# Kernel tuning notes

Measured on AMD Instinct MI355X. Metric: run time of the kernel, lower is better.

## Reference

```python
import jax, jax.numpy as jnp
import numpy as np

SINKHORN_ALPHA = 20.0
WEIGHT_LOSS_ECR = 100.0
OT_MAX_ITER = 100
STOP_THR = 0.005
EPS = 1e-16


def setup_inputs() -> dict:
    key = jax.random.key(0)
    # cost matrix: [num_topics, vocab]
    M = jax.random.uniform(key, (512, 65536), dtype=jnp.float32)
    return {"M": M}


def reference(M) -> jnp.ndarray:
    n, m = M.shape
    a = jnp.full((n, 1), 1.0 / n, dtype=M.dtype)   # row marginal
    b = jnp.full((m, 1), 1.0 / m, dtype=M.dtype)   # col marginal
    u0 = jnp.full((n, 1), 1.0 / n, dtype=M.dtype)
    K = jnp.exp(-M * SINKHORN_ALPHA)               # [n, m]

    def cond_fn(carry):
        u, v, err, cpt = carry
        return (err > STOP_THR) & (cpt < OT_MAX_ITER)

    def body_fn(carry):
        u, v, err, cpt = carry
        v = b / (K.T @ u + EPS)                    # [m, 1]
        u = a / (K @ v + EPS)                      # [n, 1]
        cpt = cpt + 1
        # convergence check every 50 iters (cpt % 50 == 1), matching torch loop
        err = jax.lax.cond(
            cpt % 50 == 1,
            lambda: jnp.sum(jnp.abs(v * (K.T @ u) - b)).astype(err.dtype),
            lambda: err,
        )
        return (u, v, err, cpt)

    init = (u0, jnp.zeros((m, 1), dtype=M.dtype), jnp.asarray(1.0, M.dtype), jnp.asarray(0, jnp.int32))
    u, v, _, _ = jax.lax.while_loop(cond_fn, body_fn, init)

    transp = u * (K * v.T)                         # [n, m] transport plan
    loss_ECR = jnp.sum(transp * M) * WEIGHT_LOSS_ECR
    return loss_ECR
```

## Files before the change

### kernel.cpp

```cpp
#include <hip/hip_runtime.h>
#include <hip/hip_cooperative_groups.h>

namespace cg = cooperative_groups;

#define NROW 512
#define NCOL 65536
#define BANDS 8
#define BPB   128

static __device__ __forceinline__ float wave_sum(float x) {
  #pragma unroll
  for (int off = 32; off; off >>= 1) x += __shfl_down(x, off, 64);
  return x;
}

__global__ __launch_bounds__(256)
void k1a_partial(const float* __restrict__ M, float* __restrict__ tPart,
                 float* __restrict__ eA) {
  const int tid = threadIdx.x, bid = blockIdx.x;
  const int band = bid >> 7, blk = bid & 127;
  const int chunk = tid & 127;
  const int part  = tid >> 7;
  const int col0  = (blk << 9) + (chunk << 2);
  const int r0    = (band << 6) + (part << 5);

  __shared__ float sCol[2 * 512];

  if (bid == 0 && tid < 3) eA[tid] = 0.f;

  float4 cs = {0.f, 0.f, 0.f, 0.f};
  #pragma unroll 8
  for (int r = r0; r < r0 + 32; ++r) {
    float4 m = *(const float4*)(M + (size_t)r * NCOL + col0);
    cs.x += __expf(-20.f * m.x);
    cs.y += __expf(-20.f * m.y);
    cs.z += __expf(-20.f * m.z);
    cs.w += __expf(-20.f * m.w);
  }
  *(float4*)(sCol + part * 512 + (chunk << 2)) = cs;
  __syncthreads();
  if (tid < 128) {
    float4 a = *(const float4*)(sCol + (tid << 2));
    float4 b = *(const float4*)(sCol + 512 + (tid << 2));
    float4 t = {a.x + b.x, a.y + b.y, a.z + b.z, a.w + b.w};
    *(float4*)(tPart + (size_t)band * NCOL + (blk << 9) + (tid << 2)) = t;
  }
}

__global__ __launch_bounds__(256)
void k1b_v1(const float* __restrict__ tPart, float* __restrict__ v) {
  const int gid = blockIdx.x * 256 + threadIdx.x;
  const int col0 = gid << 2;
  const float am = 1.0f / NROW, bm = 1.0f / NCOL, EPSV = 1e-16f;
  float4 t = {0.f, 0.f, 0.f, 0.f};
  #pragma unroll
  for (int b = 0; b < BANDS; ++b) {
    float4 p = *(const float4*)(tPart + (size_t)b * NCOL + col0);
    t.x += p.x; t.y += p.y; t.z += p.z; t.w += p.w;
  }
  float4 vv = {bm / (t.x * am + EPSV), bm / (t.y * am + EPSV),
               bm / (t.z * am + EPSV), bm / (t.w * am + EPSV)};
  *(float4*)(v + col0) = vv;
}

__global__ __launch_bounds__(256)
void k2_rowdot(const float* __restrict__ M, const float* __restrict__ v,
               float* __restrict__ u) {
  const int tid = threadIdx.x, row = blockIdx.x;
  const float am = 1.0f / NROW, EPSV = 1e-16f;
  const float4* M4 = (const float4*)M + (size_t)row * (NCOL / 4);
  const float4* V4 = (const float4*)v;
  __shared__ float sRed[4];

  float acc = 0.f;
  #pragma unroll 8
  for (int it = 0; it < NCOL / 4 / 256; ++it) {
    const int c = (it << 8) + tid;
    float4 m = M4[c];
    float4 vv = V4[c];
    acc += __expf(-20.f * m.x) * vv.x + __expf(-20.f * m.y) * vv.y
         + __expf(-20.f * m.z) * vv.z + __expf(-20.f * m.w) * vv.w;
  }
  acc = wave_sum(acc);
  if ((tid & 63) == 0) sRed[tid >> 6] = acc;
  __syncthreads();
  if (tid == 0)
    u[row] = am / (sRed[0] + sRed[1] + sRed[2] + sRed[3] + EPSV);
}

__global__ __launch_bounds__(256)
void k3a_partial(const float* __restrict__ M, const float* __restrict__ v,
                 const float* __restrict__ u, float* __restrict__ tPart,
                 float* __restrict__ eA) {
  const int tid = threadIdx.x, bid = blockIdx.x;
  const int band = bid >> 7, blk = bid & 127;
  const int chunk = tid & 127;
  const int part  = tid >> 7;
  const int col0  = (blk << 9) + (chunk << 2);
  const int r0l   = part << 5;

  __shared__ float sU[64];
  __shared__ float sCol[2 * 512];
  __shared__ float sRed[4];

  if (tid < 64) sU[tid] = u[(band << 6) + tid];
  __syncthreads();

  const float4 vv = *(const float4*)(v + col0);
  const float* Mb = M + (size_t)(band << 6) * NCOL;
  float4 cs = {0.f, 0.f, 0.f, 0.f};
  float lacc = 0.f;
  #pragma unroll 8
  for (int rl = r0l; rl < r0l + 32; ++rl) {
    float4 m = *(const float4*)(Mb + (size_t)rl * NCOL + col0);
    float e0 = __expf(-20.f * m.x), e1 = __expf(-20.f * m.y);
    float e2 = __expf(-20.f * m.z), e3 = __expf(-20.f * m.w);
    float us = sU[rl];
    cs.x = fmaf(e0, us, cs.x);
    cs.y = fmaf(e1, us, cs.y);
    cs.z = fmaf(e2, us, cs.z);
    cs.w = fmaf(e3, us, cs.w);
    lacc += us * (e0 * m.x * vv.x + e1 * m.y * vv.y
                + e2 * m.z * vv.z + e3 * m.w * vv.w);
  }
  *(float4*)(sCol + part * 512 + (chunk << 2)) = cs;
  lacc = wave_sum(lacc);
  if ((tid & 63) == 0) sRed[tid >> 6] = lacc;
  __syncthreads();
  if (tid < 128) {
    float4 a = *(const float4*)(sCol + (tid << 2));
    float4 b = *(const float4*)(sCol + 512 + (tid << 2));
    float4 t = {a.x + b.x, a.y + b.y, a.z + b.z, a.w + b.w};
    *(float4*)(tPart + (size_t)band * NCOL + (blk << 9) + (tid << 2)) = t;
  }
  if (tid == 0)
    atomicAdd(&eA[2], sRed[0] + sRed[1] + sRed[2] + sRed[3]);
}

__global__ __launch_bounds__(256)
void k3b_err(const float* __restrict__ tPart, const float* __restrict__ v,
             float* __restrict__ tArr, float* __restrict__ eA) {
  const int tid = threadIdx.x;
  const int gid = blockIdx.x * 256 + tid;
  const int col0 = gid << 2;
  const float bm = 1.0f / NCOL;
  __shared__ float sRed[4];

  float4 t = {0.f, 0.f, 0.f, 0.f};
  #pragma unroll
  for (int b = 0; b < BANDS; ++b) {
    float4 p = *(const float4*)(tPart + (size_t)b * NCOL + col0);
    t.x += p.x; t.y += p.y; t.z += p.z; t.w += p.w;
  }
  *(float4*)(tArr + col0) = t;
  float4 vv = *(const float4*)(v + col0);
  float pe = fabsf(vv.x * t.x - bm) + fabsf(vv.y * t.y - bm)
           + fabsf(vv.z * t.z - bm) + fabsf(vv.w * t.w - bm);
  pe = wave_sum(pe);
  if ((tid & 63) == 0) sRed[tid >> 6] = pe;
  __syncthreads();
  if (tid == 0)
    atomicAdd(&eA[0], sRed[0] + sRed[1] + sRed[2] + sRed[3]);
}

__global__ void k4_decide(const float* __restrict__ eA, float* __restrict__ out,
                          int* __restrict__ done) {
  if (threadIdx.x == 0) {
    if (eA[0] <= 0.005f) { out[0] = 100.f * eA[2]; done[0] = 1; }
    else                 { out[0] = 0.f;           done[0] = 0; }
  }
}

__global__ __launch_bounds__(1024)
void k5_fallback(const float* __restrict__ M, float* __restrict__ out,
                 float* __restrict__ v, float* __restrict__ u,
                 const float* __restrict__ tArr, float* __restrict__ eA,
                 const int* __restrict__ done) {
  if (done[0]) return;
  cg::grid_group grid = cg::this_grid();
  const int tid = threadIdx.x, bid = blockIdx.x;
  const float am = 1.0f / NROW, bm = 1.0f / NCOL, EPSV = 1e-16f;

  __shared__ float sU[NROW];
  __shared__ float sCol[16 * 256];
  __shared__ float sRedA[16], sRedB[16];

  const int chunk = tid & 63;
  const int part  = tid >> 6;
  const int col0  = (bid << 8) + (chunk << 2);
  const int r0    = part << 5;
  const int row0  = bid << 1;

  float tt = (tid < 256) ? tArr[(bid << 8) + tid] : 0.f;

  int cpt = 1;
  while (true) {
    if (tid < 256) v[(bid << 8) + tid] = bm / (tt + EPSV);
    grid.sync();
    cpt++;

    {
      const float4* M40 = (const float4*)M + (size_t)row0 * (NCOL / 4);
      const float4* M41 = (const float4*)M + (size_t)(row0 + 1) * (NCOL / 4);
      const float4* V4  = (const float4*)v;
      float ra = 0.f, rb = 0.f;
      #pragma unroll 4
      for (int it = 0; it < NCOL / 4 / 1024; ++it) {
        const int c = (it << 10) + tid;
        float4 vv = V4[c];
        float4 m0 = M40[c], m1 = M41[c];
        ra += __expf(-20.f * m0.x) * vv.x + __expf(-20.f * m0.y) * vv.y
            + __expf(-20.f * m0.z) * vv.z + __expf(-20.f * m0.w) * vv.w;
        rb += __expf(-20.f * m1.x) * vv.x + __expf(-20.f * m1.y) * vv.y
            + __expf(-20.f * m1.z) * vv.z + __expf(-20.f * m1.w) * vv.w;
      }
      ra = wave_sum(ra); rb = wave_sum(rb);
      if ((tid & 63) == 0) { sRedA[tid >> 6] = ra; sRedB[tid >> 6] = rb; }
      __syncthreads();
      if (tid < 2) {
        const float* sr = (tid == 0) ? sRedA : sRedB;
        float s = 0.f;
        #pragma unroll
        for (int w = 0; w < 16; ++w) s += sr[w];
        u[row0 + tid] = am / (s + EPSV);
      }
    }
    grid.sync();
    if (cpt >= 100) break;

    if (tid < NROW) sU[tid] = u[tid];
    __syncthreads();
    float4 cs = {0.f, 0.f, 0.f, 0.f};
    #pragma unroll 4
    for (int r = r0; r < r0 + 32; ++r) {
      float4 m = *(const float4*)(M + (size_t)r * NCOL + col0);
      float us = sU[r];
      cs.x = fmaf(__expf(-20.f * m.x), us, cs.x);
      cs.y = fmaf(__expf(-20.f * m.y), us, cs.y);
      cs.z = fmaf(__expf(-20.f * m.z), us, cs.z);
      cs.w = fmaf(__expf(-20.f * m.w), us, cs.w);
    }
    *(float4*)(sCol + part * 256 + (chunk << 2)) = cs;
    __syncthreads();
    if (tid < 256) {
      tt = 0.f;
      #pragma unroll
      for (int p = 0; p < 16; ++p) tt += sCol[p * 256 + tid];
    }

    if (cpt == 51) {
      float pe = (tid < 256) ? fabsf(v[(bid << 8) + tid] * tt - bm) : 0.f;
      pe = wave_sum(pe);
      __syncthreads();
      if ((tid & 63) == 0) sRedA[tid >> 6] = pe;
      __syncthreads();
      if (tid == 0) {
        float s = 0.f;
        #pragma unroll
        for (int w = 0; w < 16; ++w) s += sRedA[w];
        atomicAdd(&eA[1], s);
      }
      grid.sync();
      if (eA[1] <= 0.005f) break;
    }
  }

  __syncthreads();
  if (tid < NROW) sU[tid] = u[tid];
  __syncthreads();
  {
    const float4 vv = *(const float4*)(v + col0);
    float lacc = 0.f;
    #pragma unroll 4
    for (int r = r0; r < r0 + 32; ++r) {
      float4 m = *(const float4*)(M + (size_t)r * NCOL + col0);
      float us = sU[r];
      lacc += us * (__expf(-20.f * m.x) * m.x * vv.x
                  + __expf(-20.f * m.y) * m.y * vv.y
                  + __expf(-20.f * m.z) * m.z * vv.z
                  + __expf(-20.f * m.w) * m.w * vv.w);
    }
    lacc = wave_sum(lacc);
    if ((tid & 63) == 0) sRedA[tid >> 6] = lacc;
    __syncthreads();
    if (tid == 0) {
      float s = 0.f;
      #pragma unroll
      for (int w = 0; w < 16; ++w) s += sRedA[w];
      atomicAdd(out, 100.f * s);
    }
  }
}

extern "C" void kernel_launch(void* const* d_in, const int* in_sizes, int n_in,
                              void* d_out, int out_size, void* d_ws, size_t ws_size,
                              hipStream_t stream) {
  const float* M = (const float*)d_in[0];
  float* out = (float*)d_out;

  const size_t offV = 0;
  const size_t offT = offV + (size_t)NCOL * sizeof(float);
  const size_t offU = offT + (size_t)NCOL * sizeof(float);
  const size_t offE = offU + 4096;
  const size_t offD = offE + 256;
  const size_t offP = offD + 256;
  const size_t need = offP + (size_t)BANDS * NCOL * sizeof(float);
  if (ws_size < need) return;

  char* ws = (char*)d_ws;
  float* v     = (float*)(ws + offV);
  float* tArr  = (float*)(ws + offT);
  float* u     = (float*)(ws + offU);
  float* eA    = (float*)(ws + offE);
  int*   done  = (int*)(ws + offD);
  float* tPart = (float*)(ws + offP);

  k1a_partial<<<dim3(1024), dim3(256), 0, stream>>>(M, tPart, eA);
  k1b_v1     <<<dim3(64),   dim3(256), 0, stream>>>(tPart, v);
  k2_rowdot  <<<dim3(512),  dim3(256), 0, stream>>>(M, v, u);
  k3a_partial<<<dim3(1024), dim3(256), 0, stream>>>(M, v, u, tPart, eA);
  k3b_err    <<<dim3(64),   dim3(256), 0, stream>>>(tPart, v, tArr, eA);
  k4_decide  <<<dim3(1),    dim3(64),  0, stream>>>(eA, out, done);

  void* args[] = { (void*)&M, (void*)&out, (void*)&v, (void*)&u,
                   (void*)&tArr, (void*)&eA, (void*)&done };
  hipLaunchCooperativeKernel((void*)k5_fallback, dim3(256), dim3(1024),
                             args, 0, stream);
}
```

Measured before the change: 269.4 us.

## Fuse first Sinkhorn iteration and error check into single cooperative kernel

Replaces the six-kernel prologue (column sums, v init, row dot, partial column sums, error reduction, decide) with phases inside the single cooperative kernel, separated by grid syncs. The ECR loss partial for the early-exit case is folded into the row-dot pass, and the banded partial-sum workspace round trips are dropped. This targets launch overhead and extra global traffic in the common early-converging case. In exchange it adds grid-wide barriers and runs with only 256 blocks of 1024 threads, which may lower memory-level parallelism for the heavy M passes.

```diff
diff --git a/kernel.cpp b/kernel.cpp
--- a/kernel.cpp
+++ b/kernel.cpp
@@ -5,8 +5,6 @@
 
 #define NROW 512
 #define NCOL 65536
-#define BANDS 8
-#define BPB   128
 
 static __device__ __forceinline__ float wave_sum(float x) {
   #pragma unroll
@@ -14,176 +12,17 @@
   return x;
 }
 
-__global__ __launch_bounds__(256)
-void k1a_partial(const float* __restrict__ M, float* __restrict__ tPart,
-                 float* __restrict__ eA) {
-  const int tid = threadIdx.x, bid = blockIdx.x;
-  const int band = bid >> 7, blk = bid & 127;
-  const int chunk = tid & 127;
-  const int part  = tid >> 7;
-  const int col0  = (blk << 9) + (chunk << 2);
-  const int r0    = (band << 6) + (part << 5);
-
-  __shared__ float sCol[2 * 512];
-
-  if (bid == 0 && tid < 3) eA[tid] = 0.f;
-
-  float4 cs = {0.f, 0.f, 0.f, 0.f};
-  #pragma unroll 8
-  for (int r = r0; r < r0 + 32; ++r) {
-    float4 m = *(const float4*)(M + (size_t)r * NCOL + col0);
-    cs.x += __expf(-20.f * m.x);
-    cs.y += __expf(-20.f * m.y);
-    cs.z += __expf(-20.f * m.z);
-    cs.w += __expf(-20.f * m.w);
-  }
-  *(float4*)(sCol + part * 512 + (chunk << 2)) = cs;
-  __syncthreads();
-  if (tid < 128) {
-    float4 a = *(const float4*)(sCol + (tid << 2));
-    float4 b = *(const float4*)(sCol + 512 + (tid << 2));
-    float4 t = {a.x + b.x, a.y + b.y, a.z + b.z, a.w + b.w};
-    *(float4*)(tPart + (size_t)band * NCOL + (blk << 9) + (tid << 2)) = t;
-  }
-}
-
-__global__ __launch_bounds__(256)
-void k1b_v1(const float* __restrict__ tPart, float* __restrict__ v) {
-  const int gid = blockIdx.x * 256 + threadIdx.x;
-  const int col0 = gid << 2;
-  const float am = 1.0f / NROW, bm = 1.0f / NCOL, EPSV = 1e-16f;
-  float4 t = {0.f, 0.f, 0.f, 0.f};
-  #pragma unroll
-  for (int b = 0; b < BANDS; ++b) {
-    float4 p = *(const float4*)(tPart + (size_t)b * NCOL + col0);
-    t.x += p.x; t.y += p.y; t.z += p.z; t.w += p.w;
-  }
-  float4 vv = {bm / (t.x * am + EPSV), bm / (t.y * am + EPSV),
-               bm / (t.z * am + EPSV), bm / (t.w * am + EPSV)};
-  *(float4*)(v + col0) = vv;
-}
-
-__global__ __launch_bounds__(256)
-void k2_rowdot(const float* __restrict__ M, const float* __restrict__ v,
-               float* __restrict__ u) {
-  const int tid = threadIdx.x, row = blockIdx.x;
-  const float am = 1.0f / NROW, EPSV = 1e-16f;
-  const float4* M4 = (const float4*)M + (size_t)row * (NCOL / 4);
-  const float4* V4 = (const float4*)v;
-  __shared__ float sRed[4];
-
-  float acc = 0.f;
-  #pragma unroll 8
-  for (int it = 0; it < NCOL / 4 / 256; ++it) {
-    const int c = (it << 8) + tid;
-    float4 m = M4[c];
-    float4 vv = V4[c];
-    acc += __expf(-20.f * m.x) * vv.x + __expf(-20.f * m.y) * vv.y
-         + __expf(-20.f * m.z) * vv.z + __expf(-20.f * m.w) * vv.w;
-  }
-  acc = wave_sum(acc);
-  if ((tid & 63) == 0) sRed[tid >> 6] = acc;
-  __syncthreads();
-  if (tid == 0)
-    u[row] = am / (sRed[0] + sRed[1] + sRed[2] + sRed[3] + EPSV);
-}
-
-__global__ __launch_bounds__(256)
-void k3a_partial(const float* __restrict__ M, const float* __restrict__ v,
-                 const float* __restrict__ u, float* __restrict__ tPart,
-                 float* __restrict__ eA) {
-  const int tid = threadIdx.x, bid = blockIdx.x;
-  const int band = bid >> 7, blk = bid & 127;
-  const int chunk = tid & 127;
-  const int part  = tid >> 7;
-  const int col0  = (blk << 9) + (chunk << 2);
-  const int r0l   = part << 5;
-
-  __shared__ float sU[64];
-  __shared__ float sCol[2 * 512];
-  __shared__ float sRed[4];
-
-  if (tid < 64) sU[tid] = u[(band << 6) + tid];
-  __syncthreads();
-
-  const float4 vv = *(const float4*)(v + col0);
-  const float* Mb = M + (size_t)(band << 6) * NCOL;
-  float4 cs = {0.f, 0.f, 0.f, 0.f};
-  float lacc = 0.f;
-  #pragma unroll 8
-  for (int rl = r0l; rl < r0l + 32; ++rl) {
-    float4 m = *(const float4*)(Mb + (size_t)rl * NCOL + col0);
-    float e0 = __expf(-20.f * m.x), e1 = __expf(-20.f * m.y);
-    float e2 = __expf(-20.f * m.z), e3 = __expf(-20.f * m.w);
-    float us = sU[rl];
-    cs.x = fmaf(e0, us, cs.x);
-    cs.y = fmaf(e1, us, cs.y);
-    cs.z = fmaf(e2, us, cs.z);
-    cs.w = fmaf(e3, us, cs.w);
-    lacc += us * (e0 * m.x * vv.x + e1 * m.y * vv.y
-                + e2 * m.z * vv.z + e3 * m.w * vv.w);
-  }
-  *(float4*)(sCol + part * 512 + (chunk << 2)) = cs;
-  lacc = wave_sum(lacc);
-  if ((tid & 63) == 0) sRed[tid >> 6] = lacc;
-  __syncthreads();
-  if (tid < 128) {
-    float4 a = *(const float4*)(sCol + (tid << 2));
-    float4 b = *(const float4*)(sCol + 512 + (tid << 2));
-    float4 t = {a.x + b.x, a.y + b.y, a.z + b.z, a.w + b.w};
-    *(float4*)(tPart + (size_t)band * NCOL + (blk << 9) + (tid << 2)) = t;
-  }
-  if (tid == 0)
-    atomicAdd(&eA[2], sRed[0] + sRed[1] + sRed[2] + sRed[3]);
-}
-
-__global__ __launch_bounds__(256)
-void k3b_err(const float* __restrict__ tPart, const float* __restrict__ v,
-             float* __restrict__ tArr, float* __restrict__ eA) {
-  const int tid = threadIdx.x;
-  const int gid = blockIdx.x * 256 + tid;
-  const int col0 = gid << 2;
-  const float bm = 1.0f / NCOL;
-  __shared__ float sRed[4];
-
-  float4 t = {0.f, 0.f, 0.f, 0.f};
-  #pragma unroll
-  for (int b = 0; b < BANDS; ++b) {
-    float4 p = *(const float4*)(tPart + (size_t)b * NCOL + col0);
-    t.x += p.x; t.y += p.y; t.z += p.z; t.w += p.w;
-  }
-  *(float4*)(tArr + col0) = t;
-  float4 vv = *(const float4*)(v + col0);
-  float pe = fabsf(vv.x * t.x - bm) + fabsf(vv.y * t.y - bm)
-           + fabsf(vv.z * t.z - bm) + fabsf(vv.w * t.w - bm);
-  pe = wave_sum(pe);
-  if ((tid & 63) == 0) sRed[tid >> 6] = pe;
-  __syncthreads();
-  if (tid == 0)
-    atomicAdd(&eA[0], sRed[0] + sRed[1] + sRed[2] + sRed[3]);
-}
-
-__global__ void k4_decide(const float* __restrict__ eA, float* __restrict__ out,
-                          int* __restrict__ done) {
-  if (threadIdx.x == 0) {
-    if (eA[0] <= 0.005f) { out[0] = 100.f * eA[2]; done[0] = 1; }
-    else                 { out[0] = 0.f;           done[0] = 0; }
-  }
-}
-
 __global__ __launch_bounds__(1024)
-void k5_fallback(const float* __restrict__ M, float* __restrict__ out,
-                 float* __restrict__ v, float* __restrict__ u,
-                 const float* __restrict__ tArr, float* __restrict__ eA,
-                 const int* __restrict__ done) {
-  if (done[0]) return;
+void sinkhorn_all(const float* __restrict__ M, float* __restrict__ out,
+                  float* __restrict__ v, float* __restrict__ u,
+                  float* __restrict__ eA) {
   cg::grid_group grid = cg::this_grid();
   const int tid = threadIdx.x, bid = blockIdx.x;
   const float am = 1.0f / NROW, bm = 1.0f / NCOL, EPSV = 1e-16f;
 
+  __shared__ float sCol[16 * 256];
   __shared__ float sU[NROW];
-  __shared__ float sCol[16 * 256];
-  __shared__ float sRedA[16], sRedB[16];
+  __shared__ float sRedA[16], sRedB[16], sRedC[16], sRedD[16];
 
   const int chunk = tid & 63;
   const int part  = tid >> 6;
@@ -191,17 +30,121 @@
   const int r0    = part << 5;
   const int row0  = bid << 1;
 
-  float tt = (tid < 256) ? tArr[(bid << 8) + tid] : 0.f;
-
+  if (bid == 0 && tid < 4) eA[tid] = 0.f;
+
+  {
+    const float* Mp = M + (size_t)r0 * NCOL + col0;
+    float4 cs = {0.f, 0.f, 0.f, 0.f};
+    #pragma unroll 8
+    for (int rr = 0; rr < 32; ++rr) {
+      float4 m = *(const float4*)(Mp + (size_t)rr * NCOL);
+      cs.x += __expf(-20.f * m.x);
+      cs.y += __expf(-20.f * m.y);
+      cs.z += __expf(-20.f * m.z);
+      cs.w += __expf(-20.f * m.w);
+    }
+    *(float4*)(sCol + part * 256 + (chunk << 2)) = cs;
+    __syncthreads();
+    if (tid < 256) {
+      float t = 0.f;
+      #pragma unroll
+      for (int p = 0; p < 16; ++p) t += sCol[p * 256 + tid];
+      v[(bid << 8) + tid] = bm / (t * am + EPSV);
+    }
+  }
+  grid.sync();
+
+  {
+    const float4* M40 = (const float4*)M + (size_t)row0 * (NCOL / 4);
+    const float4* M41 = M40 + (NCOL / 4);
+    const float4* V4  = (const float4*)v;
+    float ra = 0.f, rb = 0.f, sa = 0.f, sb = 0.f;
+    #pragma unroll 4
+    for (int it = 0; it < NCOL / 4 / 1024; ++it) {
+      const int c = (it << 10) + tid;
+      float4 vv = V4[c];
+      float4 m0 = M40[c], m1 = M41[c];
+      float e;
+      e = __expf(-20.f * m0.x); ra = fmaf(e, vv.x, ra); sa = fmaf(e * m0.x, vv.x, sa);
+      e = __expf(-20.f * m0.y); ra = fmaf(e, vv.y, ra); sa = fmaf(e * m0.y, vv.y, sa);
+      e = __expf(-20.f * m0.z); ra = fmaf(e, vv.z, ra); sa = fmaf(e * m0.z, vv.z, sa);
+      e = __expf(-20.f * m0.w); ra = fmaf(e, vv.w, ra); sa = fmaf(e * m0.w, vv.w, sa);
+      e = __expf(-20.f * m1.x); rb = fmaf(e, vv.x, rb); sb = fmaf(e * m1.x, vv.x, sb);
+      e = __expf(-20.f * m1.y); rb = fmaf(e, vv.y, rb); sb = fmaf(e * m1.y, vv.y, sb);
+      e = __expf(-20.f * m1.z); rb = fmaf(e, vv.z, rb); sb = fmaf(e * m1.z, vv.z, sb);
+      e = __expf(-20.f * m1.w); rb = fmaf(e, vv.w, rb); sb = fmaf(e * m1.w, vv.w, sb);
+    }
+    ra = wave_sum(ra); rb = wave_sum(rb);
+    sa = wave_sum(sa); sb = wave_sum(sb);
+    if ((tid & 63) == 0) {
+      sRedA[tid >> 6] = ra; sRedB[tid >> 6] = rb;
+      sRedC[tid >> 6] = sa; sRedD[tid >> 6] = sb;
+    }
+    __syncthreads();
+    if (tid == 0) {
+      float rs0 = 0.f, rs1 = 0.f, ss0 = 0.f, ss1 = 0.f;
+      #pragma unroll
+      for (int w = 0; w < 16; ++w) {
+        rs0 += sRedA[w]; rs1 += sRedB[w];
+        ss0 += sRedC[w]; ss1 += sRedD[w];
+      }
+      float u0v = am / (rs0 + EPSV);
+      float u1v = am / (rs1 + EPSV);
+      u[row0] = u0v; u[row0 + 1] = u1v;
+      atomicAdd(&eA[2], u0v * ss0 + u1v * ss1);
+    }
+  }
+  grid.sync();
+
+  float tt = 0.f;
+  {
+    if (tid < NROW) sU[tid] = u[tid];
+    __syncthreads();
+    const float* Mp = M + (size_t)r0 * NCOL + col0;
+    float4 cs = {0.f, 0.f, 0.f, 0.f};
+    #pragma unroll 8
+    for (int rr = 0; rr < 32; ++rr) {
+      float4 m = *(const float4*)(Mp + (size_t)rr * NCOL);
+      float us = sU[r0 + rr];
+      cs.x = fmaf(__expf(-20.f * m.x), us, cs.x);
+      cs.y = fmaf(__expf(-20.f * m.y), us, cs.y);
+      cs.z = fmaf(__expf(-20.f * m.z), us, cs.z);
+      cs.w = fmaf(__expf(-20.f * m.w), us, cs.w);
+    }
+    *(float4*)(sCol + part * 256 + (chunk << 2)) = cs;
+    __syncthreads();
+    float pe = 0.f;
+    if (tid < 256) {
+      #pragma unroll
+      for (int p = 0; p < 16; ++p) tt += sCol[p * 256 + tid];
+      pe = fabsf(v[(bid << 8) + tid] * tt - bm);
+    }
+    pe = wave_sum(pe);
+    if ((tid & 63) == 0) sRedA[tid >> 6] = pe;
+    __syncthreads();
+    if (tid == 0) {
+      float s = 0.f;
+      #pragma unroll
+      for (int w = 0; w < 16; ++w) s += sRedA[w];
+      atomicAdd(&eA[0], s);
+    }
+  }
+  grid.sync();
+
+  if (eA[0] <= 0.005f) {
+    if (bid == 0 && tid == 0) out[0] = 100.f * eA[2];
+    return;
+  }
+
+  if (bid == 0 && tid == 0) out[0] = 0.f;
   int cpt = 1;
   while (true) {
     if (tid < 256) v[(bid << 8) + tid] = bm / (tt + EPSV);
     grid.sync();
     cpt++;
-
     {
       const float4* M40 = (const float4*)M + (size_t)row0 * (NCOL / 4);
-      const float4* M41 = (const float4*)M + (size_t)(row0 + 1) * (NCOL / 4);
+      const float4* M41 = M40 + (NCOL / 4);
       const float4* V4  = (const float4*)v;
       float ra = 0.f, rb = 0.f;
       #pragma unroll 4
@@ -217,12 +160,12 @@
       ra = wave_sum(ra); rb = wave_sum(rb);
       if ((tid & 63) == 0) { sRedA[tid >> 6] = ra; sRedB[tid >> 6] = rb; }
       __syncthreads();
-      if (tid < 2) {
-        const float* sr = (tid == 0) ? sRedA : sRedB;
-        float s = 0.f;
+      if (tid == 0) {
+        float s0 = 0.f, s1 = 0.f;
         #pragma unroll
-        for (int w = 0; w < 16; ++w) s += sr[w];
-        u[row0 + tid] = am / (s + EPSV);
+        for (int w = 0; w < 16; ++w) { s0 += sRedA[w]; s1 += sRedB[w]; }
+        u[row0]     = am / (s0 + EPSV);
+        u[row0 + 1] = am / (s1 + EPSV);
       }
     }
     grid.sync();
@@ -230,28 +173,29 @@
 
     if (tid < NROW) sU[tid] = u[tid];
     __syncthreads();
-    float4 cs = {0.f, 0.f, 0.f, 0.f};
-    #pragma unroll 4
-    for (int r = r0; r < r0 + 32; ++r) {
-      float4 m = *(const float4*)(M + (size_t)r * NCOL + col0);
-      float us = sU[r];
-      cs.x = fmaf(__expf(-20.f * m.x), us, cs.x);
-      cs.y = fmaf(__expf(-20.f * m.y), us, cs.y);
-      cs.z = fmaf(__expf(-20.f * m.z), us, cs.z);
-      cs.w = fmaf(__expf(-20.f * m.w), us, cs.w);
-    }
-    *(float4*)(sCol + part * 256 + (chunk << 2)) = cs;
-    __syncthreads();
-    if (tid < 256) {
-      tt = 0.f;
-      #pragma unroll
-      for (int p = 0; p < 16; ++p) tt += sCol[p * 256 + tid];
-    }
-
+    {
+      const float* Mp = M + (size_t)r0 * NCOL + col0;
+      float4 cs = {0.f, 0.f, 0.f, 0.f};
+      #pragma unroll 4
+      for (int rr = 0; rr < 32; ++rr) {
+        float4 m = *(const float4*)(Mp + (size_t)rr * NCOL);
+        float us = sU[r0 + rr];
+        cs.x = fmaf(__expf(-20.f * m.x), us, cs.x);
+        cs.y = fmaf(__expf(-20.f * m.y), us, cs.y);
+        cs.z = fmaf(__expf(-20.f * m.z), us, cs.z);
+        cs.w = fmaf(__expf(-20.f * m.w), us, cs.w);
+      }
+      *(float4*)(sCol + part * 256 + (chunk << 2)) = cs;
+      __syncthreads();
+      if (tid < 256) {
+        tt = 0.f;
+        #pragma unroll
+        for (int p = 0; p < 16; ++p) tt += sCol[p * 256 + tid];
+      }
+    }
     if (cpt == 51) {
       float pe = (tid < 256) ? fabsf(v[(bid << 8) + tid] * tt - bm) : 0.f;
       pe = wave_sum(pe);
-      __syncthreads();
       if ((tid & 63) == 0) sRedA[tid >> 6] = pe;
       __syncthreads();
       if (tid == 0) {
@@ -270,11 +214,12 @@
   __syncthreads();
   {
     const float4 vv = *(const float4*)(v + col0);
+    const float* Mp = M + (size_t)r0 * NCOL + col0;
     float lacc = 0.f;
     #pragma unroll 4
-    for (int r = r0; r < r0 + 32; ++r) {
-      float4 m = *(const float4*)(M + (size_t)r * NCOL + col0);
-      float us = sU[r];
+    for (int rr = 0; rr < 32; ++rr) {
+      float4 m = *(const float4*)(Mp + (size_t)rr * NCOL);
+      float us = sU[r0 + rr];
       lacc += us * (__expf(-20.f * m.x) * m.x * vv.x
                   + __expf(-20.f * m.y) * m.y * vv.y
                   + __expf(-20.f * m.z) * m.z * vv.z
@@ -299,31 +244,17 @@
   float* out = (float*)d_out;
 
   const size_t offV = 0;
-  const size_t offT = offV + (size_t)NCOL * sizeof(float);
-  const size_t offU = offT + (size_t)NCOL * sizeof(float);
+  const size_t offU = offV + (size_t)NCOL * sizeof(float);
   const size_t offE = offU + 4096;
-  const size_t offD = offE + 256;
-  const size_t offP = offD + 256;
-  const size_t need = offP + (size_t)BANDS * NCOL * sizeof(float);
+  const size_t need = offE + 256;
   if (ws_size < need) return;
 
   char* ws = (char*)d_ws;
-  float* v     = (float*)(ws + offV);
-  float* tArr  = (float*)(ws + offT);
-  float* u     = (float*)(ws + offU);
-  float* eA    = (float*)(ws + offE);
-  int*   done  = (int*)(ws + offD);
-  float* tPart = (float*)(ws + offP);
-
-  k1a_partial<<<dim3(1024), dim3(256), 0, stream>>>(M, tPart, eA);
-  k1b_v1     <<<dim3(64),   dim3(256), 0, stream>>>(tPart, v);
-  k2_rowdot  <<<dim3(512),  dim3(256), 0, stream>>>(M, v, u);
-  k3a_partial<<<dim3(1024), dim3(256), 0, stream>>>(M, v, u, tPart, eA);
-  k3b_err    <<<dim3(64),   dim3(256), 0, stream>>>(tPart, v, tArr, eA);
-  k4_decide  <<<dim3(1),    dim3(64),  0, stream>>>(eA, out, done);
-
-  void* args[] = { (void*)&M, (void*)&out, (void*)&v, (void*)&u,
-                   (void*)&tArr, (void*)&eA, (void*)&done };
-  hipLaunchCooperativeKernel((void*)k5_fallback, dim3(256), dim3(1024),
+  float* v  = (float*)(ws + offV);
+  float* u  = (float*)(ws + offU);
+  float* eA = (float*)(ws + offE);
+
+  void* args[] = { (void*)&M, (void*)&out, (void*)&v, (void*)&u, (void*)&eA };
+  hipLaunchCooperativeKernel((void*)sinkhorn_all, dim3(256), dim3(1024),
                              args, 0, stream);
 }
```

New measurement: 321.9 us. 1.19x slower.
